# Kernel optimization log

Hardware: AMD Instinct MI355X
Metric: run time of the kernel (lower is better)

The kernel has to match this reference:

```python
import jax, jax.numpy as jnp
import numpy as np
from functools import partial


def lstm(x, Wx, Wh, b, act):
    """Keras LSTM. x:[B,T,F]. Gate order i,f,c,o. Returns (all_h:[B,T,H], last_h:[B,H])."""
    B, T, _ = x.shape
    H = Wh.shape[0]
    xz = jnp.einsum('btf,fg->btg', x, Wx) + b  # precompute input projections
    def step(carry, xz_t):
        h, c = carry
        z = xz_t + h @ Wh
        i, f, g, o = jnp.split(z, 4, axis=-1)
        i = jax.nn.sigmoid(i); f = jax.nn.sigmoid(f)
        g = act(g); o = jax.nn.sigmoid(o)
        c = f * c + i * g
        h = o * act(c)
        return (h, c), h
    init = (jnp.zeros((B, H), x.dtype), jnp.zeros((B, H), x.dtype))
    (h_last, _), hs = jax.lax.scan(step, init, jnp.swapaxes(xz, 0, 1))
    return jnp.swapaxes(hs, 0, 1), h_last


def gru(x, Wx, Wh, b):
    """Keras GRU with reset_after=True. b:[2,3H]. Gate order z,r,h. Returns last h."""
    B, T, _ = x.shape
    H = Wh.shape[0]
    xz = jnp.einsum('btf,fg->btg', x, Wx) + b[0]
    def step(h, xz_t):
        rec = h @ Wh + b[1]
        xz_z, xz_r, xz_h = jnp.split(xz_t, 3, axis=-1)
        r_z, r_r, r_h = jnp.split(rec, 3, axis=-1)
        z = jax.nn.sigmoid(xz_z + r_z)
        r = jax.nn.sigmoid(xz_r + r_r)
        hh = jnp.tanh(xz_h + r * r_h)
        h = z * h + (1.0 - z) * hh
        return h, None
    h0 = jnp.zeros((B, H), x.dtype)
    h_last, _ = jax.lax.scan(step, h0, jnp.swapaxes(xz, 0, 1))
    return h_last


def setup_inputs() -> dict:
    key = jax.random.key(0)
    ks = jax.random.split(key, 32)
    s = 0.05  # small init so relu-LSTM stays numerically stable over 64 steps
    d = {}
    d['keypoint_data'] = jax.random.normal(ks[0], (256, 64, 1662), jnp.float32)
    d['img_data'] = jax.random.normal(ks[1], (256, 64, 2048), jnp.float32)
    # keypoint LSTM stack: 1662->64->128->64, gates=4H
    d['kW1x'] = s * jax.random.normal(ks[2], (1662, 256), jnp.float32)
    d['kW1h'] = s * jax.random.normal(ks[3], (64, 256), jnp.float32)
    d['kb1'] = jnp.zeros((256,), jnp.float32)
    d['kW2x'] = s * jax.random.normal(ks[4], (64, 512), jnp.float32)
    d['kW2h'] = s * jax.random.normal(ks[5], (128, 512), jnp.float32)
    d['kb2'] = jnp.zeros((512,), jnp.float32)
    d['kW3x'] = s * jax.random.normal(ks[6], (128, 256), jnp.float32)
    d['kW3h'] = s * jax.random.normal(ks[7], (64, 256), jnp.float32)
    d['kb3'] = jnp.zeros((256,), jnp.float32)
    # keypoint dense heads
    d['kD1w'] = s * jax.random.normal(ks[8], (64, 64), jnp.float32)
    d['kD1b'] = jnp.zeros((64,), jnp.float32)
    d['kD2w'] = s * jax.random.normal(ks[9], (64, 32), jnp.float32)
    d['kD2b'] = jnp.zeros((32,), jnp.float32)
    # img branch: LSTM 2048->64 (tanh), GRU 64->8 (reset_after bias [2,24])
    d['iWx'] = s * jax.random.normal(ks[10], (2048, 256), jnp.float32)
    d['iWh'] = s * jax.random.normal(ks[11], (64, 256), jnp.float32)
    d['ib'] = jnp.zeros((256,), jnp.float32)
    d['gWx'] = s * jax.random.normal(ks[12], (64, 24), jnp.float32)
    d['gWh'] = s * jax.random.normal(ks[13], (8, 24), jnp.float32)
    d['gb'] = jnp.zeros((2, 24), jnp.float32)
    d['iDw'] = s * jax.random.normal(ks[14], (8, 8), jnp.float32)
    d['iDb'] = jnp.zeros((8,), jnp.float32)
    # final dense on concat([img(8), key(32)]) -> num_classes
    d['fW'] = s * jax.random.normal(ks[15], (40, 10), jnp.float32)
    d['fb'] = jnp.zeros((10,), jnp.float32)
    return d


def reference(keypoint_data, img_data,
              kW1x, kW1h, kb1, kW2x, kW2h, kb2, kW3x, kW3h, kb3,
              kD1w, kD1b, kD2w, kD2b,
              iWx, iWh, ib, gWx, gWh, gb, iDw, iDb, fW, fb):
    relu = jax.nn.relu
    # keypoint branch: 3 relu-LSTMs
    h, _ = lstm(keypoint_data, kW1x, kW1h, kb1, relu)
    h, _ = lstm(h, kW2x, kW2h, kb2, relu)
    _, h = lstm(h, kW3x, kW3h, kb3, relu)  # return_sequences=False
    h = relu(h @ kD1w + kD1b)
    key_out = relu(h @ kD2w + kD2b)  # [B,32]
    # img branch: tanh LSTM -> GRU -> (dropout=identity at inference) -> dense
    hs, _ = lstm(img_data, iWx, iWh, ib, jnp.tanh)
    g = gru(hs, gWx, gWh, gb)  # [B,8]
    img_out = relu(g @ iDw + iDb)  # [B,8]
    combined = jnp.concatenate([img_out, key_out], axis=-1)  # [B,40]
    return jax.nn.softmax(combined @ fW + fb, axis=-1)
```

## Files before the change

kernel.cpp:

```cpp
#include <hip/hip_runtime.h>


typedef short bf16x8 __attribute__((ext_vector_type(8)));
typedef float f32x4 __attribute__((ext_vector_type(4)));

__device__ __forceinline__ unsigned f2bf(float x) {
    unsigned u = __float_as_uint(x);
    return (u + 0x7FFFu + ((u >> 16) & 1u)) >> 16;
}
__device__ __forceinline__ float bf2f(unsigned b) { return __uint_as_float(b << 16); }
__device__ __forceinline__ float sigmoidf_(float x) { return 1.f / (1.f + __expf(-x)); }
__device__ __forceinline__ float tanhf_(float x) {
    float e = __expf(2.f * x);
    return 1.f - 2.f / (e + 1.f);
}

template<int K, int N>
__device__ __forceinline__ void split_w(const float* __restrict__ W,
                                        unsigned short* __restrict__ hi,
                                        unsigned short* __restrict__ lo, int item) {
    int kt = item / N;
    int n  = item % N;
    unsigned uh[16], ul[16];
#pragma unroll
    for (int p = 0; p < 16; p++) {
        unsigned h2[2], l2[2];
#pragma unroll
        for (int e = 0; e < 2; e++) {
            int k = kt * 32 + p * 2 + e;
            float x = (k < K) ? W[(size_t)k * N + n] : 0.f;
            unsigned hb = f2bf(x);
            h2[e] = hb;
            l2[e] = f2bf(x - bf2f(hb));
        }
        uh[p] = h2[0] | (h2[1] << 16);
        ul[p] = l2[0] | (l2[1] << 16);
    }
    size_t off = (size_t)(kt * N + n) * 32;
    uint4* dh = (uint4*)(hi + off);
    uint4* dl = (uint4*)(lo + off);
#pragma unroll
    for (int c = 0; c < 4; c++) {
        uint4 v; v.x = uh[c*4]; v.y = uh[c*4+1]; v.z = uh[c*4+2]; v.w = uh[c*4+3];
        dh[c] = v;
        uint4 u; u.x = ul[c*4]; u.y = ul[c*4+1]; u.z = ul[c*4+2]; u.w = ul[c*4+3];
        dl[c] = u;
    }
}

__global__ __launch_bounds__(256) void split_all(
    const float* kW1x, const float* iWx, const float* kW2x, const float* kW3x,
    unsigned short* w1h, unsigned short* w1l, unsigned short* wih, unsigned short* wil,
    unsigned short* w2h, unsigned short* w2l, unsigned short* w3h, unsigned short* w3l) {
    int wid = blockIdx.x * 256 + threadIdx.x;
    if (wid < 13312)       split_w<1662, 256>(kW1x, w1h, w1l, wid);
    else if (wid < 29696)  split_w<2048, 256>(iWx,  wih, wil, wid - 13312);
    else if (wid < 30720)  split_w<64,   512>(kW2x, w2h, w2l, wid - 29696);
    else if (wid < 31744)  split_w<128,  256>(kW3x, w3h, w3l, wid - 30720);
}

__global__ __launch_bounds__(256, 2) void gemm_rd(
    const float* __restrict__ A, const unsigned short* __restrict__ Bhi,
    const unsigned short* __restrict__ Blo, const float* __restrict__ bias,
    float* __restrict__ out0, float* __restrict__ out1,
    int Kreal, int Kt, int Nfull) {
    const int m0  = blockIdx.x * 64;
    const int n0  = blockIdx.y * 256;
    const int ks  = blockIdx.z;
    const int nks = gridDim.z;
    const int ktChunk = Kt / nks;
    const int kt0 = ks * ktChunk;
    const int G   = ktChunk / 2;
    const int tid = threadIdx.x;
    const int lane = tid & 63;
    const int wv   = tid >> 6;
    const int l15  = lane & 15;
    const int q    = lane >> 4;
    const int row  = tid >> 2;
    const int kc   = tid & 3;

    __shared__ unsigned short Ah[2][2][64 * 40], Al[2][2][64 * 40];

    f32x4 acc[4][4];
#pragma unroll
    for (int i = 0; i < 4; i++)
#pragma unroll
        for (int j = 0; j < 4; j++) acc[i][j] = (f32x4){0.f, 0.f, 0.f, 0.f};

    auto loadA = [&](int g, float* r) {
        int kb = (kt0 + 2 * g) * 32 + kc * 16;
        const float* ap = A + (size_t)(m0 + row) * Kreal + kb;
#pragma unroll
        for (int j = 0; j < 8; j++) {
            int gk = kb + 2 * j;
            if (gk + 2 <= Kreal) {
                float2 p = *(const float2*)(ap + 2 * j);
                r[2*j] = p.x; r[2*j+1] = p.y;
            } else {
                r[2*j]   = (gk < Kreal) ? ap[2*j] : 0.f;
                r[2*j+1] = 0.f;
            }
        }
    };
    auto writeA = [&](int buf, const float* r) {
        int sub = kc >> 1;
        int kk0 = (kc & 1) * 16;
        unsigned ph[8], pl[8];
#pragma unroll
        for (int p = 0; p < 8; p++) {
            unsigned h0 = f2bf(r[2*p]),   h1 = f2bf(r[2*p+1]);
            unsigned l0 = f2bf(r[2*p] - bf2f(h0));
            unsigned l1 = f2bf(r[2*p+1] - bf2f(h1));
            ph[p] = h0 | (h1 << 16);
            pl[p] = l0 | (l1 << 16);
        }
        uint4* dh = (uint4*)&Ah[buf][sub][row * 40 + kk0];
        uint4* dl = (uint4*)&Al[buf][sub][row * 40 + kk0];
        uint4 v0; v0.x = ph[0]; v0.y = ph[1]; v0.z = ph[2]; v0.w = ph[3];
        uint4 v1; v1.x = ph[4]; v1.y = ph[5]; v1.z = ph[6]; v1.w = ph[7];
        dh[0] = v0; dh[1] = v1;
        uint4 u0; u0.x = pl[0]; u0.y = pl[1]; u0.z = pl[2]; u0.w = pl[3];
        uint4 u1; u1.x = pl[4]; u1.y = pl[5]; u1.z = pl[6]; u1.w = pl[7];
        dl[0] = u0; dl[1] = u1;
    };

    float r0[16];
    loadA(0, r0);
    writeA(0, r0);

    for (int g = 0; g < G; g++) {
        int buf = g & 1;
        __syncthreads();
        float rn[16];
        if (g + 1 < G) loadA(g + 1, rn);
#pragma unroll
        for (int sub = 0; sub < 2; sub++) {
            int ktg = kt0 + 2 * g + sub;
            bf16x8 bh[4], bl[4];
#pragma unroll
            for (int nt = 0; nt < 4; nt++) {
                size_t boff = ((size_t)ktg * Nfull + n0 + wv * 64 + nt * 16 + l15) * 32 + q * 8;
                bh[nt] = *(const bf16x8*)(Bhi + boff);
                bl[nt] = *(const bf16x8*)(Blo + boff);
            }
#pragma unroll
            for (int mt = 0; mt < 4; mt++) {
                int o = (mt * 16 + l15) * 40 + q * 8;
                bf16x8 ah = *(const bf16x8*)&Ah[buf][sub][o];
                bf16x8 al = *(const bf16x8*)&Al[buf][sub][o];
#pragma unroll
                for (int nt = 0; nt < 4; nt++) {
                    acc[mt][nt] = __builtin_amdgcn_mfma_f32_16x16x32_bf16(ah, bh[nt], acc[mt][nt], 0, 0, 0);
                    acc[mt][nt] = __builtin_amdgcn_mfma_f32_16x16x32_bf16(ah, bl[nt], acc[mt][nt], 0, 0, 0);
                    acc[mt][nt] = __builtin_amdgcn_mfma_f32_16x16x32_bf16(al, bh[nt], acc[mt][nt], 0, 0, 0);
                }
            }
        }
        if (g + 1 < G) writeA(buf ^ 1, rn);
    }
    float* op = (ks == 0) ? out0 : out1;
#pragma unroll
    for (int nt = 0; nt < 4; nt++) {
        int gcol = n0 + wv * 64 + nt * 16 + l15;
        float bv = (ks == 0) ? bias[gcol] : 0.f;
#pragma unroll
        for (int mt = 0; mt < 4; mt++)
#pragma unroll
            for (int r = 0; r < 4; r++) {
                int grow = m0 + mt * 16 + q * 4 + r;
                op[(size_t)grow * Nfull + gcol] = acc[mt][nt][r] + bv;
            }
    }
}

__global__ __launch_bounds__(256) void lstm_h64(
    int nA,
    const float* __restrict__ xA0, const float* __restrict__ xA1,
    const float* __restrict__ WhA, float* __restrict__ hA, int actA,
    const float* __restrict__ xB0, const float* __restrict__ xB1,
    const float* __restrict__ WhB, float* __restrict__ hB, int actB) {
    int bid = blockIdx.x;
    bool sec = bid >= nA;
    int b = sec ? bid - nA : bid;
    const float* x0 = sec ? xB0 : xA0;
    const float* x1 = sec ? xB1 : xA1;
    const float* Wh = sec ? WhB : WhA;
    float* hout     = sec ? hB  : hA;
    int act         = sec ? actB : actA;
    bool has1 = (x1 != nullptr);

    int g = threadIdx.x;
    float w[64];
#pragma unroll
    for (int k = 0; k < 64; k++) w[k] = Wh[k * 256 + g];

    __shared__ alignas(16) float hs[64];
    __shared__ float za[256];
    if (g < 64) hs[g] = 0.f;
    float c = 0.f;
    __syncthreads();

    const float* x0r = x0 + (size_t)b * 64 * 256;
    const float* x1r = has1 ? x1 + (size_t)b * 64 * 256 : x0r;
    float* hr = hout + (size_t)b * 64 * 64;
    bool isc = (g >= 128) && (g < 192);
    float cur = x0r[g] + (has1 ? x1r[g] : 0.f);
    for (int t = 0; t < 64; t++) {
        float nxt = 0.f;
        if (t < 63) {
            nxt = x0r[(t + 1) * 256 + g];
            if (has1) nxt += x1r[(t + 1) * 256 + g];
        }
        float z0 = cur, z1 = 0.f, z2 = 0.f, z3 = 0.f;
#pragma unroll
        for (int kk = 0; kk < 16; kk++) {
            float4 h4 = *(const float4*)&hs[kk * 4];
            z0 = fmaf(h4.x, w[kk * 4 + 0], z0);
            z1 = fmaf(h4.y, w[kk * 4 + 1], z1);
            z2 = fmaf(h4.z, w[kk * 4 + 2], z2);
            z3 = fmaf(h4.w, w[kk * 4 + 3], z3);
        }
        float z = (z0 + z1) + (z2 + z3);
        float a;
        if (isc) a = (act == 0) ? fmaxf(z, 0.f) : tanhf_(z);
        else     a = sigmoidf_(z);
        za[g] = a;
        __syncthreads();
        if (g < 64) {
            float iv = za[g], fv = za[64 + g], cd = za[128 + g], ov = za[192 + g];
            c = fmaf(fv, c, iv * cd);
            float ca = (act == 0) ? fmaxf(c, 0.f) : tanhf_(c);
            float h = ov * ca;
            hs[g] = h;
            hr[t * 64 + g] = h;
        }
        __syncthreads();
        cur = nxt;
    }
}

__global__ __launch_bounds__(512, 2) void lstm_h128(
    const float* __restrict__ xz, const float* __restrict__ Wh, float* __restrict__ hout) {
    int b = blockIdx.x;
    int g = threadIdx.x;
    float w[128];
#pragma unroll
    for (int k = 0; k < 128; k++) w[k] = Wh[k * 512 + g];

    __shared__ alignas(16) float hs[128];
    __shared__ float za[512];
    if (g < 128) hs[g] = 0.f;
    float c = 0.f;
    __syncthreads();

    const float* xzr = xz + (size_t)b * 64 * 512;
    float* hr = hout + (size_t)b * 64 * 128;
    bool isc = (g >= 256) && (g < 384);
    float cur = xzr[g];
    for (int t = 0; t < 64; t++) {
        float nxt = 0.f;
        if (t < 63) nxt = xzr[(t + 1) * 512 + g];
        float z0 = cur, z1 = 0.f, z2 = 0.f, z3 = 0.f;
#pragma unroll
        for (int kk = 0; kk < 32; kk++) {
            float4 h4 = *(const float4*)&hs[kk * 4];
            z0 = fmaf(h4.x, w[kk * 4 + 0], z0);
            z1 = fmaf(h4.y, w[kk * 4 + 1], z1);
            z2 = fmaf(h4.z, w[kk * 4 + 2], z2);
            z3 = fmaf(h4.w, w[kk * 4 + 3], z3);
        }
        float z = (z0 + z1) + (z2 + z3);
        float a = isc ? fmaxf(z, 0.f) : sigmoidf_(z);
        za[g] = a;
        __syncthreads();
        if (g < 128) {
            float iv = za[g], fv = za[128 + g], cd = za[256 + g], ov = za[384 + g];
            c = fmaf(fv, c, iv * cd);
            float h = ov * fmaxf(c, 0.f);
            hs[g] = h;
            hr[t * 128 + g] = h;
        }
        __syncthreads();
        cur = nxt;
    }
}

__global__ __launch_bounds__(64) void gru_kernel(
    const float* __restrict__ hsimg, const float* __restrict__ gWx,
    const float* __restrict__ gWh, const float* __restrict__ gb,
    float* __restrict__ glast) {
    int b = blockIdx.x;
    int qq = threadIdx.x;
    int col = (qq < 24) ? qq : 0;
    float wx[64], wh[8];
#pragma unroll
    for (int k = 0; k < 64; k++) wx[k] = gWx[k * 24 + col];
#pragma unroll
    for (int k = 0; k < 8; k++)  wh[k] = gWh[k * 24 + col];
    float b0 = gb[col], b1 = gb[24 + col];

    float hval = 0.f;
    const float* hb = hsimg + (size_t)b * 64 * 64;
    float cur = hb[qq];
    for (int t = 0; t < 64; t++) {
        float nxt = (t < 63) ? hb[(t + 1) * 64 + qq] : 0.f;
        float s0 = b0, s1 = 0.f, s2 = 0.f, s3 = 0.f;
#pragma unroll
        for (int k = 0; k < 64; k += 4) {
            s0 = fmaf(__shfl(cur, k + 0), wx[k + 0], s0);
            s1 = fmaf(__shfl(cur, k + 1), wx[k + 1], s1);
            s2 = fmaf(__shfl(cur, k + 2), wx[k + 2], s2);
            s3 = fmaf(__shfl(cur, k + 3), wx[k + 3], s3);
        }
        float sx = (s0 + s1) + (s2 + s3);
        float sr = b1;
#pragma unroll
        for (int k = 0; k < 8; k++) sr = fmaf(__shfl(hval, k), wh[k], sr);
        float xzz = __shfl(sx, qq),      rzz = __shfl(sr, qq);
        float xzr = __shfl(sx, 8 + qq),  rzr = __shfl(sr, 8 + qq);
        float xzh = __shfl(sx, 16 + qq), rzh = __shfl(sr, 16 + qq);
        float zz = sigmoidf_(xzz + rzz);
        float rv = sigmoidf_(xzr + rzr);
        float hc = tanhf_(xzh + rv * rzh);
        hval = zz * hval + (1.f - zz) * hc;
        cur = nxt;
    }
    if (qq < 8) glast[b * 8 + qq] = hval;
}

__global__ __launch_bounds__(64) void final_head(
    const float* __restrict__ h3seq, const float* __restrict__ glast,
    const float* __restrict__ kD1w, const float* __restrict__ kD1b,
    const float* __restrict__ kD2w, const float* __restrict__ kD2b,
    const float* __restrict__ iDw,  const float* __restrict__ iDb,
    const float* __restrict__ fW,   const float* __restrict__ fb,
    float* __restrict__ outp) {
    int b = blockIdx.x * 64 + threadIdx.x;
    float h3[64];
#pragma unroll
    for (int k = 0; k < 64; k++) h3[k] = h3seq[((size_t)b * 64 + 63) * 64 + k];
    float d1[64];
#pragma unroll
    for (int j = 0; j < 64; j++) {
        float s = kD1b[j];
#pragma unroll
        for (int k = 0; k < 64; k++) s = fmaf(h3[k], kD1w[k * 64 + j], s);
        d1[j] = fmaxf(s, 0.f);
    }
    float d2[32];
#pragma unroll
    for (int j = 0; j < 32; j++) {
        float s = kD2b[j];
#pragma unroll
        for (int k = 0; k < 64; k++) s = fmaf(d1[k], kD2w[k * 32 + j], s);
        d2[j] = fmaxf(s, 0.f);
    }
    float gi[8];
#pragma unroll
    for (int k = 0; k < 8; k++) gi[k] = glast[b * 8 + k];
    float io[8];
#pragma unroll
    for (int j = 0; j < 8; j++) {
        float s = iDb[j];
#pragma unroll
        for (int k = 0; k < 8; k++) s = fmaf(gi[k], iDw[k * 8 + j], s);
        io[j] = fmaxf(s, 0.f);
    }
    float lg[10];
#pragma unroll
    for (int j = 0; j < 10; j++) {
        float s = fb[j];
#pragma unroll
        for (int k = 0; k < 8; k++)  s = fmaf(io[k], fW[k * 10 + j], s);
#pragma unroll
        for (int k = 0; k < 32; k++) s = fmaf(d2[k], fW[(8 + k) * 10 + j], s);
        lg[j] = s;
    }
    float mx = lg[0];
#pragma unroll
    for (int j = 1; j < 10; j++) mx = fmaxf(mx, lg[j]);
    float den = 0.f, ex[10];
#pragma unroll
    for (int j = 0; j < 10; j++) { ex[j] = __expf(lg[j] - mx); den += ex[j]; }
    float inv = 1.f / den;
#pragma unroll
    for (int j = 0; j < 10; j++) outp[b * 10 + j] = ex[j] * inv;
}

extern "C" void kernel_launch(void* const* d_in, const int* in_sizes, int n_in,
                              void* d_out, int out_size, void* d_ws, size_t ws_size,
                              hipStream_t stream) {
    const float* keypoint = (const float*)d_in[0];
    const float* img      = (const float*)d_in[1];
    const float* kW1x = (const float*)d_in[2];
    const float* kW1h = (const float*)d_in[3];
    const float* kb1  = (const float*)d_in[4];
    const float* kW2x = (const float*)d_in[5];
    const float* kW2h = (const float*)d_in[6];
    const float* kb2  = (const float*)d_in[7];
    const float* kW3x = (const float*)d_in[8];
    const float* kW3h = (const float*)d_in[9];
    const float* kb3  = (const float*)d_in[10];
    const float* kD1w = (const float*)d_in[11];
    const float* kD1b = (const float*)d_in[12];
    const float* kD2w = (const float*)d_in[13];
    const float* kD2b = (const float*)d_in[14];
    const float* iWx  = (const float*)d_in[15];
    const float* iWh  = (const float*)d_in[16];
    const float* ib   = (const float*)d_in[17];
    const float* gWx  = (const float*)d_in[18];
    const float* gWh  = (const float*)d_in[19];
    const float* gb   = (const float*)d_in[20];
    const float* iDw  = (const float*)d_in[21];
    const float* iDb  = (const float*)d_in[22];
    const float* fW   = (const float*)d_in[23];
    const float* fb   = (const float*)d_in[24];
    float* outp = (float*)d_out;

    char* ws = (char*)d_ws;
    const size_t MB16 = (size_t)16384 * 256 * 4;
    float* r1a = (float*)(ws);
    float* r1b = (float*)(ws + MB16);
    float* r2a = (float*)(ws + 2 * MB16);
    float* r2b = (float*)(ws + 3 * MB16);
    size_t off = 4 * MB16;
    float* h1seq = (float*)(ws + off); off += (size_t)16384 * 64 * 4;
    float* h2seq = (float*)(ws + off); off += (size_t)16384 * 128 * 4;
    float* hsimg = (float*)(ws + off); off += (size_t)16384 * 64 * 4;
    float* glast = (float*)(ws + off); off += (size_t)256 * 8 * 4;
    unsigned short* w1h = (unsigned short*)(ws + off); off += (size_t)52 * 256 * 32 * 2;
    unsigned short* w1l = (unsigned short*)(ws + off); off += (size_t)52 * 256 * 32 * 2;
    unsigned short* wih = (unsigned short*)(ws + off); off += (size_t)64 * 256 * 32 * 2;
    unsigned short* wil = (unsigned short*)(ws + off); off += (size_t)64 * 256 * 32 * 2;
    unsigned short* w2h = (unsigned short*)(ws + off); off += (size_t)2 * 512 * 32 * 2;
    unsigned short* w2l = (unsigned short*)(ws + off); off += (size_t)2 * 512 * 32 * 2;
    unsigned short* w3h = (unsigned short*)(ws + off); off += (size_t)4 * 256 * 32 * 2;
    unsigned short* w3l = (unsigned short*)(ws + off); off += (size_t)4 * 256 * 32 * 2;
    float* xz2   = r2a;
    float* h3seq = h1seq;

    split_all<<<124, 256, 0, stream>>>(kW1x, iWx, kW2x, kW3x,
                                       w1h, w1l, wih, wil, w2h, w2l, w3h, w3l);
    gemm_rd<<<dim3(256, 1, 2), 256, 0, stream>>>(keypoint, w1h, w1l, kb1, r1a, r1b, 1662, 52, 256);
    gemm_rd<<<dim3(256, 1, 2), 256, 0, stream>>>(img, wih, wil, ib, r2a, r2b, 2048, 64, 256);
    lstm_h64<<<512, 256, 0, stream>>>(256, r1a, r1b, kW1h, h1seq, 0, r2a, r2b, iWh, hsimg, 1);
    gemm_rd<<<dim3(256, 2, 1), 256, 0, stream>>>(h1seq, w2h, w2l, kb2, xz2, xz2, 64, 2, 512);
    lstm_h128<<<256, 512, 0, stream>>>(xz2, kW2h, h2seq);
    gemm_rd<<<dim3(256, 1, 2), 256, 0, stream>>>(h2seq, w3h, w3l, kb3, r1a, r1b, 128, 4, 256);
    lstm_h64<<<256, 256, 0, stream>>>(256, r1a, r1b, kW3h, h3seq, 0, r1a, r1b, kW3h, h3seq, 0);
    gru_kernel<<<256, 64, 0, stream>>>(hsimg, gWx, gWh, gb, glast);
    final_head<<<4, 64, 0, stream>>>(h3seq, glast, kD1w, kD1b, kD2w, kD2b,
                                     iDw, iDb, fW, fb, outp);
    (void)in_sizes; (void)n_in; (void)out_size; (void)ws_size;
}
```

Before: 700.3 us.

## Restructure split-bf16 GEMM to load A directly into registers, drop LDS staging

The input-projection GEMM no longer stages the fp32 A tile through double-buffered shared memory with barriers. Each wave now owns 16 rows across all 256 columns, loads its A fragment straight from global memory into registers, and converts it to hi/lo bf16 per k-tile. B fragments are streamed and software-pipelined in halves between MFMA groups. This removes LDS traffic and __syncthreads, but every wave now reads all B columns (4x more B global/L2 traffic per block) and A loads are less coalesced, with a higher register footprint from 16 accumulators.

```diff
diff --git a/kernel.cpp b/kernel.cpp
--- a/kernel.cpp
+++ b/kernel.cpp
@@ -59,117 +59,122 @@
     else if (wid < 31744)  split_w<128,  256>(kW3x, w3h, w3l, wid - 30720);
 }
 
-__global__ __launch_bounds__(256, 2) void gemm_rd(
+__global__ __launch_bounds__(256, 2) void gemm_bf(
     const float* __restrict__ A, const unsigned short* __restrict__ Bhi,
     const unsigned short* __restrict__ Blo, const float* __restrict__ bias,
     float* __restrict__ out0, float* __restrict__ out1,
     int Kreal, int Kt, int Nfull) {
-    const int m0  = blockIdx.x * 64;
-    const int n0  = blockIdx.y * 256;
-    const int ks  = blockIdx.z;
-    const int nks = gridDim.z;
-    const int ktChunk = Kt / nks;
+    const int m0 = blockIdx.x * 64;
+    const int n0 = blockIdx.y * 256;
+    const int ks = blockIdx.z;
+    const int ktChunk = (Kt + gridDim.z - 1) / gridDim.z;
     const int kt0 = ks * ktChunk;
-    const int G   = ktChunk / 2;
-    const int tid = threadIdx.x;
+    const int ktEnd = min(Kt, kt0 + ktChunk);
+    const int tid  = threadIdx.x;
     const int lane = tid & 63;
     const int wv   = tid >> 6;
     const int l15  = lane & 15;
     const int q    = lane >> 4;
-    const int row  = tid >> 2;
-    const int kc   = tid & 3;
-
-    __shared__ unsigned short Ah[2][2][64 * 40], Al[2][2][64 * 40];
-
-    f32x4 acc[4][4];
-#pragma unroll
-    for (int i = 0; i < 4; i++)
-#pragma unroll
-        for (int j = 0; j < 4; j++) acc[i][j] = (f32x4){0.f, 0.f, 0.f, 0.f};
-
-    auto loadA = [&](int g, float* r) {
-        int kb = (kt0 + 2 * g) * 32 + kc * 16;
-        const float* ap = A + (size_t)(m0 + row) * Kreal + kb;
-#pragma unroll
-        for (int j = 0; j < 8; j++) {
+
+    const float* arow = A + (size_t)(m0 + wv * 16 + l15) * Kreal;
+    const int lp = l15 * 32 + q * 8;
+
+    f32x4 acc[16];
+#pragma unroll
+    for (int i = 0; i < 16; i++) acc[i] = (f32x4){0.f, 0.f, 0.f, 0.f};
+
+    float af[2][8];
+    auto loadA = [&](int kt, float* r) {
+        int kb = kt * 32 + q * 8;
+#pragma unroll
+        for (int j = 0; j < 4; j++) {
             int gk = kb + 2 * j;
+            float x0 = 0.f, x1 = 0.f;
             if (gk + 2 <= Kreal) {
-                float2 p = *(const float2*)(ap + 2 * j);
-                r[2*j] = p.x; r[2*j+1] = p.y;
-            } else {
-                r[2*j]   = (gk < Kreal) ? ap[2*j] : 0.f;
-                r[2*j+1] = 0.f;
+                float2 p = *(const float2*)(arow + gk);
+                x0 = p.x; x1 = p.y;
+            } else if (gk < Kreal) {
+                x0 = arow[gk];
             }
+            r[2*j] = x0; r[2*j+1] = x1;
         }
     };
-    auto writeA = [&](int buf, const float* r) {
-        int sub = kc >> 1;
-        int kk0 = (kc & 1) * 16;
-        unsigned ph[8], pl[8];
-#pragma unroll
-        for (int p = 0; p < 8; p++) {
-            unsigned h0 = f2bf(r[2*p]),   h1 = f2bf(r[2*p+1]);
+    union BF8 { unsigned u[4]; bf16x8 v; };
+    auto conv = [&](const float* r, bf16x8& ah, bf16x8& al) {
+        BF8 H, L;
+#pragma unroll
+        for (int p = 0; p < 4; p++) {
+            unsigned h0 = f2bf(r[2*p]), h1 = f2bf(r[2*p+1]);
             unsigned l0 = f2bf(r[2*p] - bf2f(h0));
             unsigned l1 = f2bf(r[2*p+1] - bf2f(h1));
-            ph[p] = h0 | (h1 << 16);
-            pl[p] = l0 | (l1 << 16);
-        }
-        uint4* dh = (uint4*)&Ah[buf][sub][row * 40 + kk0];
-        uint4* dl = (uint4*)&Al[buf][sub][row * 40 + kk0];
-        uint4 v0; v0.x = ph[0]; v0.y = ph[1]; v0.z = ph[2]; v0.w = ph[3];
-        uint4 v1; v1.x = ph[4]; v1.y = ph[5]; v1.z = ph[6]; v1.w = ph[7];
-        dh[0] = v0; dh[1] = v1;
-        uint4 u0; u0.x = pl[0]; u0.y = pl[1]; u0.z = pl[2]; u0.w = pl[3];
-        uint4 u1; u1.x = pl[4]; u1.y = pl[5]; u1.z = pl[6]; u1.w = pl[7];
-        dl[0] = u0; dl[1] = u1;
+            H.u[p] = h0 | (h1 << 16);
+            L.u[p] = l0 | (l1 << 16);
+        }
+        ah = H.v; al = L.v;
     };
 
-    float r0[16];
-    loadA(0, r0);
-    writeA(0, r0);
-
-    for (int g = 0; g < G; g++) {
-        int buf = g & 1;
-        __syncthreads();
-        float rn[16];
-        if (g + 1 < G) loadA(g + 1, rn);
-#pragma unroll
-        for (int sub = 0; sub < 2; sub++) {
-            int ktg = kt0 + 2 * g + sub;
-            bf16x8 bh[4], bl[4];
-#pragma unroll
-            for (int nt = 0; nt < 4; nt++) {
-                size_t boff = ((size_t)ktg * Nfull + n0 + wv * 64 + nt * 16 + l15) * 32 + q * 8;
-                bh[nt] = *(const bf16x8*)(Bhi + boff);
-                bl[nt] = *(const bf16x8*)(Blo + boff);
+    loadA(kt0, af[0]);
+    if (kt0 + 1 < ktEnd) loadA(kt0 + 1, af[1]);
+
+    bf16x8 bh[2][4], bl[2][4];
+    for (int kt = kt0; kt < ktEnd; kt++) {
+        const unsigned short* bhp = Bhi + (size_t)kt * Nfull * 32 + n0 * 32 + lp;
+        const unsigned short* blp = Blo + (size_t)kt * Nfull * 32 + n0 * 32 + lp;
+#pragma unroll
+        for (int c = 0; c < 2; c++)
+#pragma unroll
+            for (int i = 0; i < 4; i++) {
+                bh[c][i] = *(const bf16x8*)(bhp + (c * 4 + i) * 512);
+                bl[c][i] = *(const bf16x8*)(blp + (c * 4 + i) * 512);
             }
-#pragma unroll
-            for (int mt = 0; mt < 4; mt++) {
-                int o = (mt * 16 + l15) * 40 + q * 8;
-                bf16x8 ah = *(const bf16x8*)&Ah[buf][sub][o];
-                bf16x8 al = *(const bf16x8*)&Al[buf][sub][o];
-#pragma unroll
-                for (int nt = 0; nt < 4; nt++) {
-                    acc[mt][nt] = __builtin_amdgcn_mfma_f32_16x16x32_bf16(ah, bh[nt], acc[mt][nt], 0, 0, 0);
-                    acc[mt][nt] = __builtin_amdgcn_mfma_f32_16x16x32_bf16(ah, bl[nt], acc[mt][nt], 0, 0, 0);
-                    acc[mt][nt] = __builtin_amdgcn_mfma_f32_16x16x32_bf16(al, bh[nt], acc[mt][nt], 0, 0, 0);
-                }
-            }
-        }
-        if (g + 1 < G) writeA(buf ^ 1, rn);
+        bf16x8 ah, al;
+        conv(af[(kt - kt0) & 1], ah, al);
+#pragma unroll
+        for (int i = 0; i < 4; i++) {
+            acc[i] = __builtin_amdgcn_mfma_f32_16x16x32_bf16(ah, bh[0][i], acc[i], 0, 0, 0);
+            acc[i] = __builtin_amdgcn_mfma_f32_16x16x32_bf16(ah, bl[0][i], acc[i], 0, 0, 0);
+            acc[i] = __builtin_amdgcn_mfma_f32_16x16x32_bf16(al, bh[0][i], acc[i], 0, 0, 0);
+        }
+#pragma unroll
+        for (int i = 0; i < 4; i++) {
+            bh[0][i] = *(const bf16x8*)(bhp + (8 + i) * 512);
+            bl[0][i] = *(const bf16x8*)(blp + (8 + i) * 512);
+        }
+#pragma unroll
+        for (int i = 0; i < 4; i++) {
+            acc[4+i] = __builtin_amdgcn_mfma_f32_16x16x32_bf16(ah, bh[1][i], acc[4+i], 0, 0, 0);
+            acc[4+i] = __builtin_amdgcn_mfma_f32_16x16x32_bf16(ah, bl[1][i], acc[4+i], 0, 0, 0);
+            acc[4+i] = __builtin_amdgcn_mfma_f32_16x16x32_bf16(al, bh[1][i], acc[4+i], 0, 0, 0);
+        }
+#pragma unroll
+        for (int i = 0; i < 4; i++) {
+            bh[1][i] = *(const bf16x8*)(bhp + (12 + i) * 512);
+            bl[1][i] = *(const bf16x8*)(blp + (12 + i) * 512);
+        }
+        if (kt + 2 < ktEnd) loadA(kt + 2, af[(kt - kt0) & 1]);
+#pragma unroll
+        for (int i = 0; i < 4; i++) {
+            acc[8+i] = __builtin_amdgcn_mfma_f32_16x16x32_bf16(ah, bh[0][i], acc[8+i], 0, 0, 0);
+            acc[8+i] = __builtin_amdgcn_mfma_f32_16x16x32_bf16(ah, bl[0][i], acc[8+i], 0, 0, 0);
+            acc[8+i] = __builtin_amdgcn_mfma_f32_16x16x32_bf16(al, bh[0][i], acc[8+i], 0, 0, 0);
+        }
+#pragma unroll
+        for (int i = 0; i < 4; i++) {
+            acc[12+i] = __builtin_amdgcn_mfma_f32_16x16x32_bf16(ah, bh[1][i], acc[12+i], 0, 0, 0);
+            acc[12+i] = __builtin_amdgcn_mfma_f32_16x16x32_bf16(ah, bl[1][i], acc[12+i], 0, 0, 0);
+            acc[12+i] = __builtin_amdgcn_mfma_f32_16x16x32_bf16(al, bh[1][i], acc[12+i], 0, 0, 0);
+        }
     }
     float* op = (ks == 0) ? out0 : out1;
 #pragma unroll
-    for (int nt = 0; nt < 4; nt++) {
-        int gcol = n0 + wv * 64 + nt * 16 + l15;
+    for (int nt = 0; nt < 16; nt++) {
+        int gcol = n0 + nt * 16 + l15;
         float bv = (ks == 0) ? bias[gcol] : 0.f;
 #pragma unroll
-        for (int mt = 0; mt < 4; mt++)
-#pragma unroll
-            for (int r = 0; r < 4; r++) {
-                int grow = m0 + mt * 16 + q * 4 + r;
-                op[(size_t)grow * Nfull + gcol] = acc[mt][nt][r] + bv;
-            }
+        for (int r = 0; r < 4; r++) {
+            int grow = m0 + wv * 16 + q * 4 + r;
+            op[(size_t)grow * Nfull + gcol] = acc[nt][r] + bv;
+        }
     }
 }
 
@@ -441,12 +446,12 @@
 
     split_all<<<124, 256, 0, stream>>>(kW1x, iWx, kW2x, kW3x,
                                        w1h, w1l, wih, wil, w2h, w2l, w3h, w3l);
-    gemm_rd<<<dim3(256, 1, 2), 256, 0, stream>>>(keypoint, w1h, w1l, kb1, r1a, r1b, 1662, 52, 256);
-    gemm_rd<<<dim3(256, 1, 2), 256, 0, stream>>>(img, wih, wil, ib, r2a, r2b, 2048, 64, 256);
+    gemm_bf<<<dim3(256, 1, 2), 256, 0, stream>>>(keypoint, w1h, w1l, kb1, r1a, r1b, 1662, 52, 256);
+    gemm_bf<<<dim3(256, 1, 2), 256, 0, stream>>>(img, wih, wil, ib, r2a, r2b, 2048, 64, 256);
     lstm_h64<<<512, 256, 0, stream>>>(256, r1a, r1b, kW1h, h1seq, 0, r2a, r2b, iWh, hsimg, 1);
-    gemm_rd<<<dim3(256, 2, 1), 256, 0, stream>>>(h1seq, w2h, w2l, kb2, xz2, xz2, 64, 2, 512);
+    gemm_bf<<<dim3(256, 2, 1), 256, 0, stream>>>(h1seq, w2h, w2l, kb2, xz2, xz2, 64, 2, 512);
     lstm_h128<<<256, 512, 0, stream>>>(xz2, kW2h, h2seq);
-    gemm_rd<<<dim3(256, 1, 2), 256, 0, stream>>>(h2seq, w3h, w3l, kb3, r1a, r1b, 128, 4, 256);
+    gemm_bf<<<dim3(256, 1, 2), 256, 0, stream>>>(h2seq, w3h, w3l, kb3, r1a, r1b, 128, 4, 256);
     lstm_h64<<<256, 256, 0, stream>>>(256, r1a, r1b, kW3h, h3seq, 0, r1a, r1b, kW3h, h3seq, 0);
     gru_kernel<<<256, 64, 0, stream>>>(hsimg, gWx, gWh, gb, glast);
     final_head<<<4, 64, 0, stream>>>(h3seq, glast, kD1w, kD1b, kD2w, kD2b,
```

Measured after the change: 850.1 us. 21.4% more time.
